# Kernel optimization log

Measured on AMD Instinct MI355X. Metric: run time of the kernel, lower is better.

Reference implementation:

```python
import jax, jax.numpy as jnp
import numpy as np

P, IMG, CH, DM, NL = 16, 224, 3, 512, 6
DI, N, K, R = 2 * DM, 16, 4, DM // 16  # d_inner, d_state, d_conv, dt_rank
BATCH = 32
L = (IMG // P) ** 2
PD = CH * P * P


def layernorm(x, g, b, eps=1e-5):
    mu = x.mean(-1, keepdims=True)
    var = x.var(-1, keepdims=True)
    return (x - mu) / jnp.sqrt(var + eps) * g + b


def mamba_layer(x, inW, convW, convB, xpW, dtW, dtB, A_log, Dvec, outW):
    # x: (B, L, DM)
    Bsz, Ls, _ = x.shape
    xz = x @ inW.T                      # (B, L, 2*DI), in_proj (bias=False)
    xs, z = jnp.split(xz, 2, axis=-1)   # (B, L, DI) each
    # causal depthwise conv1d (kernel K, left pad K-1, truncate to L)
    xp = jnp.pad(xs, ((0, 0), (K - 1, 0), (0, 0)))
    xc = sum(convW[:, k] * xp[:, k:k + Ls, :] for k in range(K)) + convB
    xc = jax.nn.silu(xc)
    # input-dependent dt, B, C
    x_dbl = xc @ xpW.T                  # (B, L, R + 2N)
    dt, Bm, Cm = jnp.split(x_dbl, [R, R + N], axis=-1)
    dt = jax.nn.softplus(dt @ dtW.T + dtB)  # (B, L, DI)
    A = -jnp.exp(A_log)                 # (DI, N)

    def step(h, inp):
        xt, dtt, Bt, Ct = inp           # (B,DI),(B,DI),(B,N),(B,N)
        dA = jnp.exp(dtt[:, :, None] * A)              # (B, DI, N)
        h = dA * h + dtt[:, :, None] * Bt[:, None, :] * xt[:, :, None]
        y = jnp.einsum('bdn,bn->bd', h, Ct)
        return h, y

    h0 = jnp.zeros((Bsz, DI, N), xs.dtype)
    xs_t = jnp.swapaxes(xc, 0, 1)
    dt_t = jnp.swapaxes(dt, 0, 1)
    B_t = jnp.swapaxes(Bm, 0, 1)
    C_t = jnp.swapaxes(Cm, 0, 1)
    _, ys = jax.lax.scan(step, h0, (xs_t, dt_t, B_t, C_t))
    y = jnp.swapaxes(ys, 0, 1) + xc * Dvec   # skip term D*x
    y = y * jax.nn.silu(z)
    return y @ outW.T                    # out_proj (bias=False)


def setup_inputs() -> dict:
    key = jax.random.key(0)
    ks = jax.random.split(key, 16)
    s = 0.02
    inp = {
        'x': jax.random.normal(ks[0], (BATCH, CH, IMG, IMG), jnp.float32),
        'ln0_g': jnp.ones((PD,), jnp.float32),
        'ln0_b': jnp.zeros((PD,), jnp.float32),
        'W_emb': jax.random.normal(ks[1], (DM, PD), jnp.float32) * s,
        'b_emb': jnp.zeros((DM,), jnp.float32),
        'ln1_g': jnp.ones((DM,), jnp.float32),
        'ln1_b': jnp.zeros((DM,), jnp.float32),
        'in_proj_w': jax.random.normal(ks[2], (NL, 2 * DI, DM), jnp.float32) * s,
        'conv_w': jax.random.normal(ks[3], (NL, DI, K), jnp.float32) * 0.1,
        'conv_b': jnp.zeros((NL, DI), jnp.float32),
        'x_proj_w': jax.random.normal(ks[4], (NL, R + 2 * N, DI), jnp.float32) * s,
        'dt_proj_w': jax.random.normal(ks[5], (NL, DI, R), jnp.float32) * s,
        'dt_proj_b': jnp.full((NL, DI), float(np.log(np.expm1(0.01))), jnp.float32),
        'A_log': jnp.tile(jnp.log(jnp.arange(1, N + 1, dtype=jnp.float32)), (NL, DI, 1)),
        'D_p': jnp.ones((NL, DI), jnp.float32),
        'out_proj_w': jax.random.normal(ks[6], (NL, DM, DI), jnp.float32) * s,
        'blk_ln_g': jnp.ones((NL, DM), jnp.float32),
        'blk_ln_b': jnp.zeros((NL, DM), jnp.float32),
        'W_head': jax.random.normal(ks[7], (10, DM), jnp.float32) * s,
        'b_head': jnp.zeros((10,), jnp.float32),
    }
    return inp


def reference(x, ln0_g, ln0_b, W_emb, b_emb, ln1_g, ln1_b, in_proj_w, conv_w,
              conv_b, x_proj_w, dt_proj_w, dt_proj_b, A_log, D_p, out_proj_w,
              blk_ln_g, blk_ln_b, W_head, b_head):
    B = x.shape[0]
    # patchify: b c (h p1) (w p2) -> b (h w) (c p1 p2)
    g = IMG // P
    t = x.reshape(B, CH, g, P, g, P).transpose(0, 2, 4, 1, 3, 5).reshape(B, g * g, PD)
    t = layernorm(t, ln0_g, ln0_b)
    t = t @ W_emb.T + b_emb
    t = layernorm(t, ln1_g, ln1_b)
    for i in range(NL):
        y = mamba_layer(t, in_proj_w[i], conv_w[i], conv_b[i], x_proj_w[i],
                        dt_proj_w[i], dt_proj_b[i], A_log[i], D_p[i], out_proj_w[i])
        t = layernorm(y + t, blk_ln_g[i], blk_ln_b[i])
    pooled = t.mean(axis=1)
    return pooled @ W_head.T + b_head
```

## Files before the change

kernel.cpp:

```cpp
#include <hip/hip_runtime.h>
#include <cstdint>
#include <cstddef>

#define BATCHN 32
#define LSEQ   196
#define DMODEL 512
#define DINNER 1024
#define PDIM   768
#define NSTATE 16
#define RRANK  32
#define NLAYER 6

typedef __bf16 bf16_t;
typedef __bf16 bf16x8 __attribute__((ext_vector_type(8)));
typedef float  f32x4  __attribute__((ext_vector_type(4)));

__device__ __forceinline__ void gl_lds16(const bf16_t* g, bf16_t* l) {
    __builtin_amdgcn_global_load_lds(
        (const __attribute__((address_space(1))) void*)g,
        (__attribute__((address_space(3))) void*)l, 16, 0, 0);
}

__global__ __launch_bounds__(256) void split_kernel(
    const float* __restrict__ src, bf16_t* __restrict__ hi,
    bf16_t* __restrict__ lo, int n)
{
    int i = blockIdx.x * 256 + threadIdx.x;
    if (i < n) {
        float x = src[i];
        bf16_t h = (bf16_t)x;
        hi[i] = h;
        lo[i] = (bf16_t)(x - (float)h);
    }
}

__global__ __launch_bounds__(256) void gemm_mfma3(
    const bf16_t* __restrict__ Ah, const bf16_t* __restrict__ Al,
    const bf16_t* __restrict__ Wh, const bf16_t* __restrict__ Wl,
    float* __restrict__ C, const float* __restrict__ bias,
    int M, int N, int K)
{
    __shared__ bf16_t sAh[128 * 32];
    __shared__ bf16_t sAl[128 * 32];
    __shared__ bf16_t sBh[128 * 32];
    __shared__ bf16_t sBl[128 * 32];

    const int bm = blockIdx.y * 128;
    const int bn = blockIdx.x * 128;
    const int tid  = threadIdx.x;
    const int lane = tid & 63;
    const int w    = tid >> 6;
    const int wm   = (w & 1) * 64;
    const int wn   = (w >> 1) * 64;

    const int lrow = lane >> 2;
    const int cg8  = ((lane & 3) ^ ((lane >> 3) & 3)) * 8;
    const size_t arow = (size_t)(bm + w * 32 + lrow) * K + cg8;
    const size_t brow = (size_t)(bn + w * 32 + lrow) * K + cg8;

    const int fsw = ((lane >> 4) ^ ((lane >> 1) & 3)) * 8;
    const int fr  = lane & 15;

    f32x4 acc[4][4] = {};

    for (int k0 = 0; k0 < K; k0 += 32) {
        __syncthreads();
        #pragma unroll
        for (int j = 0; j < 2; ++j) {
            const size_t ga = arow + (size_t)j * 16 * K + k0;
            const size_t gb = brow + (size_t)j * 16 * K + k0;
            const int lo = w * 1024 + j * 512;
            gl_lds16(Ah + ga, &sAh[lo]);
            gl_lds16(Al + ga, &sAl[lo]);
            gl_lds16(Wh + gb, &sBh[lo]);
            gl_lds16(Wl + gb, &sBl[lo]);
        }
        __syncthreads();

        bf16x8 afh[4], afl[4];
        #pragma unroll
        for (int mt = 0; mt < 4; ++mt) {
            const int r = wm + mt * 16 + fr;
            afh[mt] = *(const bf16x8*)&sAh[r * 32 + fsw];
            afl[mt] = *(const bf16x8*)&sAl[r * 32 + fsw];
        }
        #pragma unroll
        for (int nt = 0; nt < 4; ++nt) {
            const int r = wn + nt * 16 + fr;
            bf16x8 bfh = *(const bf16x8*)&sBh[r * 32 + fsw];
            bf16x8 bfl = *(const bf16x8*)&sBl[r * 32 + fsw];
            #pragma unroll
            for (int mt = 0; mt < 4; ++mt) {
                acc[mt][nt] = __builtin_amdgcn_mfma_f32_16x16x32_bf16(
                    afh[mt], bfh, acc[mt][nt], 0, 0, 0);
                acc[mt][nt] = __builtin_amdgcn_mfma_f32_16x16x32_bf16(
                    afh[mt], bfl, acc[mt][nt], 0, 0, 0);
                acc[mt][nt] = __builtin_amdgcn_mfma_f32_16x16x32_bf16(
                    afl[mt], bfh, acc[mt][nt], 0, 0, 0);
            }
        }
    }

    const int cr = (lane >> 4) * 4;
    const int cc = lane & 15;
    #pragma unroll
    for (int nt = 0; nt < 4; ++nt) {
        const int n = bn + wn + nt * 16 + cc;
        const float bv = bias ? bias[n] : 0.f;
        #pragma unroll
        for (int mt = 0; mt < 4; ++mt) {
            const int m0 = bm + wm + mt * 16 + cr;
            #pragma unroll
            for (int r = 0; r < 4; ++r)
                C[(size_t)(m0 + r) * N + n] = acc[mt][nt][r] + bv;
        }
    }
}

__global__ __launch_bounds__(256) void gemm_nt(
    const float* __restrict__ A, int lda,
    const float* __restrict__ W,
    float* __restrict__ C, int ldc,
    const float* __restrict__ bias,
    int M, int N, int K, int act)
{
    __shared__ float As[16][64];
    __shared__ float Ws[16][64];
    const int bm = blockIdx.y * 64;
    const int bn = blockIdx.x * 64;
    const int tid = threadIdx.x;
    const int tx = tid & 15;
    const int ty = tid >> 4;
    const int r   = tid >> 2;
    const int kk4 = (tid & 3) << 2;

    float acc[4][4];
    #pragma unroll
    for (int i = 0; i < 4; ++i)
        #pragma unroll
        for (int j = 0; j < 4; ++j) acc[i][j] = 0.f;

    for (int k0 = 0; k0 < K; k0 += 16) {
        float4 va = *(const float4*)(A + (size_t)(bm + r) * lda + k0 + kk4);
        float4 vw = *(const float4*)(W + (size_t)(bn + r) * K   + k0 + kk4);
        __syncthreads();
        As[kk4 + 0][r] = va.x; As[kk4 + 1][r] = va.y;
        As[kk4 + 2][r] = va.z; As[kk4 + 3][r] = va.w;
        Ws[kk4 + 0][r] = vw.x; Ws[kk4 + 1][r] = vw.y;
        Ws[kk4 + 2][r] = vw.z; Ws[kk4 + 3][r] = vw.w;
        __syncthreads();
        #pragma unroll
        for (int kk = 0; kk < 16; ++kk) {
            float4 a = *(const float4*)&As[kk][ty << 2];
            float4 b = *(const float4*)&Ws[kk][tx << 2];
            acc[0][0] += a.x * b.x; acc[0][1] += a.x * b.y;
            acc[0][2] += a.x * b.z; acc[0][3] += a.x * b.w;
            acc[1][0] += a.y * b.x; acc[1][1] += a.y * b.y;
            acc[1][2] += a.y * b.z; acc[1][3] += a.y * b.w;
            acc[2][0] += a.z * b.x; acc[2][1] += a.z * b.y;
            acc[2][2] += a.z * b.z; acc[2][3] += a.z * b.w;
            acc[3][0] += a.w * b.x; acc[3][1] += a.w * b.y;
            acc[3][2] += a.w * b.z; acc[3][3] += a.w * b.w;
        }
    }

    #pragma unroll
    for (int i = 0; i < 4; ++i) {
        const int m = bm + (ty << 2) + i;
        #pragma unroll
        for (int j = 0; j < 4; ++j) {
            const int n = bn + (tx << 2) + j;
            float v = acc[i][j];
            if (bias) v += bias[n];
            if (act == 1) {
                v = (v > 20.f) ? v : log1pf(expf(v));
            }
            C[(size_t)m * ldc + n] = v;
        }
    }
}

__global__ __launch_bounds__(256) void gemm_nt_splitk(
    const float* __restrict__ A, int lda,
    const float* __restrict__ W, int ldw,
    float* __restrict__ Cpart, int ldc,
    int M, int N, int kchunk)
{
    __shared__ float As[16][64];
    __shared__ float Ws[16][64];
    const int bm = blockIdx.y * 64;
    const int bn = blockIdx.x * 64;
    const int kb = blockIdx.z * kchunk;
    Cpart += (size_t)blockIdx.z * M * ldc;

    const int tid = threadIdx.x;
    const int tx = tid & 15;
    const int ty = tid >> 4;
    const int r   = tid >> 2;
    const int kk4 = (tid & 3) << 2;

    float acc[4][4];
    #pragma unroll
    for (int i = 0; i < 4; ++i)
        #pragma unroll
        for (int j = 0; j < 4; ++j) acc[i][j] = 0.f;

    for (int k0 = kb; k0 < kb + kchunk; k0 += 16) {
        float4 va = *(const float4*)(A + (size_t)(bm + r) * lda + k0 + kk4);
        float4 vw = *(const float4*)(W + (size_t)(bn + r) * ldw + k0 + kk4);
        __syncthreads();
        As[kk4 + 0][r] = va.x; As[kk4 + 1][r] = va.y;
        As[kk4 + 2][r] = va.z; As[kk4 + 3][r] = va.w;
        Ws[kk4 + 0][r] = vw.x; Ws[kk4 + 1][r] = vw.y;
        Ws[kk4 + 2][r] = vw.z; Ws[kk4 + 3][r] = vw.w;
        __syncthreads();
        #pragma unroll
        for (int kk = 0; kk < 16; ++kk) {
            float4 a = *(const float4*)&As[kk][ty << 2];
            float4 b = *(const float4*)&Ws[kk][tx << 2];
            acc[0][0] += a.x * b.x; acc[0][1] += a.x * b.y;
            acc[0][2] += a.x * b.z; acc[0][3] += a.x * b.w;
            acc[1][0] += a.y * b.x; acc[1][1] += a.y * b.y;
            acc[1][2] += a.y * b.z; acc[1][3] += a.y * b.w;
            acc[2][0] += a.z * b.x; acc[2][1] += a.z * b.y;
            acc[2][2] += a.z * b.z; acc[2][3] += a.z * b.w;
            acc[3][0] += a.w * b.x; acc[3][1] += a.w * b.y;
            acc[3][2] += a.w * b.z; acc[3][3] += a.w * b.w;
        }
    }

    #pragma unroll
    for (int i = 0; i < 4; ++i) {
        const int m = bm + (ty << 2) + i;
        #pragma unroll
        for (int j = 0; j < 4; ++j) {
            const int n = bn + (tx << 2) + j;
            Cpart[(size_t)m * ldc + n] = acc[i][j];
        }
    }
}

__global__ __launch_bounds__(256) void reduce_splitk(
    const float* __restrict__ part, float* __restrict__ out, int n, int nsplit)
{
    int i = blockIdx.x * 256 + threadIdx.x;
    if (i < n) {
        float s = 0.f;
        for (int j = 0; j < nsplit; ++j) s += part[(size_t)j * n + i];
        out[i] = s;
    }
}

__global__ __launch_bounds__(256) void patchify_kernel(
    const float* __restrict__ x, float* __restrict__ tp)
{
    int idx = blockIdx.x * 256 + threadIdx.x;
    int pd = idx % PDIM;
    int bl = idx / PDIM;
    int l = bl % LSEQ, b = bl / LSEQ;
    int c = pd >> 8, rem = pd & 255, p1 = rem >> 4, p2 = rem & 15;
    int gh = l / 14, gw = l % 14;
    int hh = gh * 16 + p1, ww = gw * 16 + p2;
    tp[idx] = x[(((size_t)b * 3 + c) * 224 + hh) * 224 + ww];
}

__global__ __launch_bounds__(256) void ln_kernel(
    const float* __restrict__ in, const float* __restrict__ res,
    const float* __restrict__ g, const float* __restrict__ bt,
    float* __restrict__ out, bf16_t* __restrict__ hi,
    bf16_t* __restrict__ lo, int W)
{
    __shared__ float red[4];
    const int row = blockIdx.x;
    const size_t base = (size_t)row * W;
    const int nper = W >> 8;
    float vals[3];
    float s = 0.f;
    for (int j = 0; j < nper; ++j) {
        int c = (j << 8) + threadIdx.x;
        float v = in[base + c];
        if (res) v += res[base + c];
        vals[j] = v;
        s += v;
    }
    int lane = threadIdx.x & 63, wid = threadIdx.x >> 6;
    #pragma unroll
    for (int o = 32; o > 0; o >>= 1) s += __shfl_down(s, o);
    if (lane == 0) red[wid] = s;
    __syncthreads();
    float mu = (red[0] + red[1] + red[2] + red[3]) / (float)W;
    __syncthreads();
    float vs = 0.f;
    for (int j = 0; j < nper; ++j) { float d = vals[j] - mu; vs += d * d; }
    #pragma unroll
    for (int o = 32; o > 0; o >>= 1) vs += __shfl_down(vs, o);
    if (lane == 0) red[wid] = vs;
    __syncthreads();
    float var = (red[0] + red[1] + red[2] + red[3]) / (float)W;
    float rstd = rsqrtf(var + 1e-5f);
    for (int j = 0; j < nper; ++j) {
        int c = (j << 8) + threadIdx.x;
        float v = (vals[j] - mu) * rstd * g[c] + bt[c];
        if (out) out[base + c] = v;
        if (hi) {
            bf16_t h = (bf16_t)v;
            hi[base + c] = h;
            lo[base + c] = (bf16_t)(v - (float)h);
        }
    }
}

__global__ __launch_bounds__(256) void conv_silu_kernel(
    const float* __restrict__ xz, const float* __restrict__ cw,
    const float* __restrict__ cb, float* __restrict__ xc)
{
    int idx = blockIdx.x * 256 + threadIdx.x;
    int d4 = idx & 255;
    int bl = idx >> 8;
    int l = bl % LSEQ, b = bl / LSEQ;
    int d = d4 << 2;

    float4 w0 = *(const float4*)(cw + (size_t)(d + 0) * 4);
    float4 w1 = *(const float4*)(cw + (size_t)(d + 1) * 4);
    float4 w2 = *(const float4*)(cw + (size_t)(d + 2) * 4);
    float4 w3 = *(const float4*)(cw + (size_t)(d + 3) * 4);
    float4 acc = *(const float4*)(cb + d);

    const float* base = xz + ((size_t)(b * LSEQ) << 11) + d;
    #pragma unroll
    for (int k = 0; k < 4; ++k) {
        int ls = l + k - 3;
        if (ls >= 0) {
            float4 xv = *(const float4*)(base + ((size_t)ls << 11));
            const float wk0 = (&w0.x)[k], wk1 = (&w1.x)[k];
            const float wk2 = (&w2.x)[k], wk3 = (&w3.x)[k];
            acc.x += wk0 * xv.x; acc.y += wk1 * xv.y;
            acc.z += wk2 * xv.z; acc.w += wk3 * xv.w;
        }
    }
    acc.x = acc.x * __builtin_amdgcn_rcpf(1.f + __expf(-acc.x));
    acc.y = acc.y * __builtin_amdgcn_rcpf(1.f + __expf(-acc.y));
    acc.z = acc.z * __builtin_amdgcn_rcpf(1.f + __expf(-acc.z));
    acc.w = acc.w * __builtin_amdgcn_rcpf(1.f + __expf(-acc.w));
    *(float4*)(xc + ((size_t)bl << 10) + d) = acc;
}

template<int J>
__device__ __forceinline__ float qbcast(float v) {
    constexpr int ctrl = J | (J << 2) | (J << 4) | (J << 6);
    return __int_as_float(__builtin_amdgcn_mov_dpp(
        __float_as_int(v), ctrl, 0xF, 0xF, true));
}

__global__ __launch_bounds__(256, 1) void scan_kernel(
    const float* __restrict__ xc, const float* __restrict__ dt,
    const float* __restrict__ xdbl, const float* __restrict__ A_log,
    const float* __restrict__ Dv, const float* __restrict__ xz,
    bf16_t* __restrict__ yh, bf16_t* __restrict__ yl)
{
    __shared__ float sBC[4][2][256];

    const int b    = blockIdx.y;
    const int tid  = threadIdx.x;
    const int lane = tid & 63;
    const int w    = tid >> 6;
    const int q    = tid >> 2;
    const int sub  = tid & 3;
    const int d    = blockIdx.x * 64 + q;

    float A2[4], h[4];
    #pragma unroll
    for (int n = 0; n < 4; ++n) {
        A2[n] = -__expf(A_log[d * NSTATE + sub * 4 + n]) * 1.44269504f;
        h[n] = 0.f;
    }
    const float Dval = Dv[d];
    const size_t bL = (size_t)b * LSEQ;

    const float* pdt = dt + (bL + sub) * DINNER + d;
    const float* pxc = xc + (bL + sub) * DINNER + d;
    const float* pz  = xz + ((bL + sub) << 11) + DINNER + d;

    const float* xrow = xdbl + bL * 64;
    const int roff = (lane >> 4) * 64 + (lane & 15) * 4;
    float* lds0 = &sBC[w][0][0];
    float* lds1 = &sBC[w][1][0];

    float4 r0 = *(const float4*)(xrow + roff);
    float4 r1 = *(const float4*)(xrow + 256 + roff);
    float4 rowreg = *(const float4*)(xrow + 512 + roff);
    *(float4*)(lds0 + roff) = r0;
    *(float4*)(lds1 + roff) = r1;

    float dt_c = pdt[0];          float xc_c = pxc[0];          float z_c = pz[0];
    float dt_1 = pdt[4 * DINNER]; float xc_1 = pxc[4 * DINNER]; float z_1 = pz[4 * 2048];

    for (int g = 0; g < 49; ++g) {
        const int gl  = (g + 3 <= 48) ? g + 3 : 48;
        float4 rownext = *(const float4*)(xrow + gl * 256 + roff);
        const int adv = (g < 47) ? 2 : (48 - g);
        float dt_2 = pdt[(size_t)adv * 4 * DINNER];
        float xc_2 = pxc[(size_t)adv * 4 * DINNER];
        float z_2  = pz[(size_t)adv * 4 * 2048];

        const float* Bbuf = (g & 1) ? lds1 : lds0;
        float acc_keep = 0.f;

#define SCAN_STEP(J) do {                                                     \
        float4 Bv = *(const float4*)&Bbuf[(J) * 64 + 32 + 4 * sub];           \
        float4 Cv = *(const float4*)&Bbuf[(J) * 64 + 48 + 4 * sub];           \
        float dtv = qbcast<J>(dt_c);                                          \
        float xv  = qbcast<J>(xc_c);                                          \
        float dtx = dtv * xv;                                                 \
        h[0] = exp2f(dtv * A2[0]) * h[0] + dtx * Bv.x;                        \
        h[1] = exp2f(dtv * A2[1]) * h[1] + dtx * Bv.y;                        \
        h[2] = exp2f(dtv * A2[2]) * h[2] + dtx * Bv.z;                        \
        h[3] = exp2f(dtv * A2[3]) * h[3] + dtx * Bv.w;                        \
        float acc = h[0] * Cv.x + h[1] * Cv.y + h[2] * Cv.z + h[3] * Cv.w;    \
        acc += __shfl_xor(acc, 1);                                            \
        acc += __shfl_xor(acc, 2);                                            \
        acc_keep = (sub == (J)) ? acc : acc_keep;                             \
    } while (0)

        SCAN_STEP(0);
        SCAN_STEP(1);
        SCAN_STEP(2);
        SCAN_STEP(3);
#undef SCAN_STEP

        {
            float yv = acc_keep + xc_c * Dval;
            float sz = z_c * __builtin_amdgcn_rcpf(1.f + __expf(-z_c));
            float o  = yv * sz;
            bf16_t ho = (bf16_t)o;
            const size_t oi = (bL + 4 * (size_t)g + sub) * DINNER + d;
            yh[oi] = ho;
            yl[oi] = (bf16_t)(o - (float)ho);
        }

        *(float4*)(((g & 1) ? lds1 : lds0) + roff) = rowreg;
        rowreg = rownext;

        pdt += 4 * DINNER; pxc += 4 * DINNER; pz += 4 * 2048;
        dt_c = dt_1; xc_c = xc_1; z_c = z_1;
        dt_1 = dt_2; xc_1 = xc_2; z_1 = z_2;
    }
}

__global__ __launch_bounds__(256) void pool_kernel(
    const float* __restrict__ t, float* __restrict__ pooled)
{
    int idx = blockIdx.x * 256 + threadIdx.x;
    int dm = idx & (DMODEL - 1);
    int b = idx >> 9;
    float s = 0.f;
    for (int l = 0; l < LSEQ; ++l)
        s += t[((size_t)(b * LSEQ + l) << 9) + dm];
    pooled[idx] = s * (1.f / (float)LSEQ);
}

__global__ __launch_bounds__(320) void head_kernel(
    const float* __restrict__ pooled, const float* __restrict__ Wh,
    const float* __restrict__ bh, float* __restrict__ out)
{
    int tid = threadIdx.x;
    if (tid >= 320) return;
    int b = tid / 10, o = tid % 10;
    float s = bh[o];
    for (int k = 0; k < DMODEL; ++k)
        s += pooled[b * DMODEL + k] * Wh[o * DMODEL + k];
    out[b * 10 + o] = s;
}

extern "C" void kernel_launch(void* const* d_in, const int* in_sizes, int n_in,
                              void* d_out, int out_size, void* d_ws, size_t ws_size,
                              hipStream_t stream)
{
    const float* x         = (const float*)d_in[0];
    const float* ln0_g     = (const float*)d_in[1];
    const float* ln0_b     = (const float*)d_in[2];
    const float* W_emb     = (const float*)d_in[3];
    const float* b_emb     = (const float*)d_in[4];
    const float* ln1_g     = (const float*)d_in[5];
    const float* ln1_b     = (const float*)d_in[6];
    const float* in_proj_w = (const float*)d_in[7];
    const float* conv_w    = (const float*)d_in[8];
    const float* conv_b    = (const float*)d_in[9];
    const float* x_proj_w  = (const float*)d_in[10];
    const float* dt_proj_w = (const float*)d_in[11];
    const float* dt_proj_b = (const float*)d_in[12];
    const float* A_log     = (const float*)d_in[13];
    const float* D_p       = (const float*)d_in[14];
    const float* out_proj_w= (const float*)d_in[15];
    const float* blk_ln_g  = (const float*)d_in[16];
    const float* blk_ln_b  = (const float*)d_in[17];
    const float* W_head    = (const float*)d_in[18];
    const float* b_head    = (const float*)d_in[19];

    const int M = BATCHN * LSEQ;
    const int NSPLIT = 8;

    char* ws = (char*)d_ws;
    size_t off = 0;
    auto alloc = [&](size_t bytes) -> void* {
        void* p = (void*)(ws + off);
        off += (bytes + 255) & ~(size_t)255;
        return p;
    };
    float*  tp     = (float*)alloc((size_t)M * PDIM * 4);
    bf16_t* tp_h   = (bf16_t*)alloc((size_t)M * PDIM * 2);
    bf16_t* tp_l   = (bf16_t*)alloc((size_t)M * PDIM * 2);
    float*  t      = (float*)alloc((size_t)M * DMODEL * 4);
    bf16_t* t_h    = (bf16_t*)alloc((size_t)M * DMODEL * 2);
    bf16_t* t_l    = (bf16_t*)alloc((size_t)M * DMODEL * 2);
    float*  xz     = (float*)alloc((size_t)M * 2 * DINNER * 4);
    float*  xc     = (float*)alloc((size_t)M * DINNER * 4);
    float*  xdbl   = (float*)alloc((size_t)M * 64 * 4);
    float*  xdbl_p = (float*)alloc((size_t)NSPLIT * M * 64 * 4);
    float*  dtbuf  = (float*)alloc((size_t)M * DINNER * 4);
    bf16_t* y_h    = (bf16_t*)alloc((size_t)M * DINNER * 2);
    bf16_t* y_l    = (bf16_t*)alloc((size_t)M * DINNER * 2);
    float*  yout   = (float*)alloc((size_t)M * DMODEL * 4);
    float*  pooled = (float*)alloc((size_t)BATCHN * DMODEL * 4);
    const int n_inW  = NLAYER * 2 * DINNER * DMODEL;
    const int n_outW = NLAYER * DMODEL * DINNER;
    const int n_embW = DMODEL * PDIM;
    bf16_t* winh  = (bf16_t*)alloc((size_t)n_inW * 2);
    bf16_t* winl  = (bf16_t*)alloc((size_t)n_inW * 2);
    bf16_t* wouth = (bf16_t*)alloc((size_t)n_outW * 2);
    bf16_t* woutl = (bf16_t*)alloc((size_t)n_outW * 2);
    bf16_t* wembh = (bf16_t*)alloc((size_t)n_embW * 2);
    bf16_t* wembl = (bf16_t*)alloc((size_t)n_embW * 2);
    (void)ws_size; (void)in_sizes; (void)n_in; (void)out_size;

    split_kernel<<<(n_inW  + 255) / 256, 256, 0, stream>>>(in_proj_w,  winh,  winl,  n_inW);
    split_kernel<<<(n_outW + 255) / 256, 256, 0, stream>>>(out_proj_w, wouth, woutl, n_outW);
    split_kernel<<<(n_embW + 255) / 256, 256, 0, stream>>>(W_emb,      wembh, wembl, n_embW);

    patchify_kernel<<<(M * PDIM) / 256, 256, 0, stream>>>(x, tp);
    ln_kernel<<<M, 256, 0, stream>>>(tp, nullptr, ln0_g, ln0_b, nullptr, tp_h, tp_l, PDIM);
    gemm_mfma3<<<dim3(DMODEL / 128, M / 128), 256, 0, stream>>>(
        tp_h, tp_l, wembh, wembl, t, b_emb, M, DMODEL, PDIM);
    ln_kernel<<<M, 256, 0, stream>>>(t, nullptr, ln1_g, ln1_b, t, t_h, t_l, DMODEL);

    for (int i = 0; i < NLAYER; ++i) {
        const bf16_t* winh_i  = winh  + (size_t)i * 2 * DINNER * DMODEL;
        const bf16_t* winl_i  = winl  + (size_t)i * 2 * DINNER * DMODEL;
        const bf16_t* wouth_i = wouth + (size_t)i * DMODEL * DINNER;
        const bf16_t* woutl_i = woutl + (size_t)i * DMODEL * DINNER;
        const float* cw   = conv_w    + (size_t)i * DINNER * 4;
        const float* cb   = conv_b    + (size_t)i * DINNER;
        const float* xpW  = x_proj_w  + (size_t)i * 64 * DINNER;
        const float* dtW  = dt_proj_w + (size_t)i * DINNER * RRANK;
        const float* dtB  = dt_proj_b + (size_t)i * DINNER;
        const float* Ali  = A_log     + (size_t)i * DINNER * NSTATE;
        const float* Di   = D_p       + (size_t)i * DINNER;
        const float* bg   = blk_ln_g  + (size_t)i * DMODEL;
        const float* bb   = blk_ln_b  + (size_t)i * DMODEL;

        gemm_mfma3<<<dim3((2 * DINNER) / 128, M / 128), 256, 0, stream>>>(
            t_h, t_l, winh_i, winl_i, xz, nullptr, M, 2 * DINNER, DMODEL);
        conv_silu_kernel<<<(M * DINNER / 4) / 256, 256, 0, stream>>>(xz, cw, cb, xc);
        gemm_nt_splitk<<<dim3(1, M / 64, NSPLIT), 256, 0, stream>>>(
            xc, DINNER, xpW, DINNER, xdbl_p, 64, M, 64, DINNER / NSPLIT);
        reduce_splitk<<<(M * 64 + 255) / 256, 256, 0, stream>>>(
            xdbl_p, xdbl, M * 64, NSPLIT);
        gemm_nt<<<dim3(DINNER / 64, M / 64), 256, 0, stream>>>(
            xdbl, 64, dtW, dtbuf, DINNER, dtB, M, DINNER, RRANK, 1);
        scan_kernel<<<dim3(DINNER / 64, BATCHN), 256, 0, stream>>>(
            xc, dtbuf, xdbl, Ali, Di, xz, y_h, y_l);
        gemm_mfma3<<<dim3(DMODEL / 128, M / 128), 256, 0, stream>>>(
            y_h, y_l, wouth_i, woutl_i, yout, nullptr, M, DMODEL, DINNER);
        ln_kernel<<<M, 256, 0, stream>>>(yout, t, bg, bb, t, t_h, t_l, DMODEL);
    }

    pool_kernel<<<(BATCHN * DMODEL) / 256, 256, 0, stream>>>(t, pooled);
    head_kernel<<<1, 320, 0, stream>>>(pooled, W_head, b_head, (float*)d_out);
}
```

Baseline: 1.697 ms.

## Fuse conv into x_proj, split-K out_proj, double-buffer GEMM B tiles

Merges the causal depthwise conv and SiLU into the split-K x_proj GEMM, which removes a separate kernel launch and one reread of xc. The out_proj GEMM now runs split-K over two z-slices, and the following layernorm sums the two partial outputs. The MFMA GEMM double-buffers only its weight tiles in LDS while the A tiles stay single-buffered behind an extra barrier. Buffers are aliased (xdbl_p onto tp, yout onto dtbuf) to save memory; the aliasing and the partially double-buffered pipeline carry correctness risk.

```diff
diff --git a/kernel.cpp b/kernel.cpp
--- a/kernel.cpp
+++ b/kernel.cpp
@@ -42,11 +42,15 @@
 {
     __shared__ bf16_t sAh[128 * 32];
     __shared__ bf16_t sAl[128 * 32];
-    __shared__ bf16_t sBh[128 * 32];
-    __shared__ bf16_t sBl[128 * 32];
+    __shared__ bf16_t sBh[2][128 * 32];
+    __shared__ bf16_t sBl[2][128 * 32];
 
     const int bm = blockIdx.y * 128;
     const int bn = blockIdx.x * 128;
+    const int kchunk = K / gridDim.z;
+    const int kb = blockIdx.z * kchunk;
+    C += (size_t)blockIdx.z * M * N;
+
     const int tid  = threadIdx.x;
     const int lane = tid & 63;
     const int w    = tid >> 6;
@@ -60,21 +64,21 @@
 
     const int fsw = ((lane >> 4) ^ ((lane >> 1) & 3)) * 8;
     const int fr  = lane & 15;
+    const int llo = w * 1024;
 
     f32x4 acc[4][4] = {};
 
-    for (int k0 = 0; k0 < K; k0 += 32) {
-        __syncthreads();
-        #pragma unroll
-        for (int j = 0; j < 2; ++j) {
-            const size_t ga = arow + (size_t)j * 16 * K + k0;
-            const size_t gb = brow + (size_t)j * 16 * K + k0;
-            const int lo = w * 1024 + j * 512;
-            gl_lds16(Ah + ga, &sAh[lo]);
-            gl_lds16(Al + ga, &sAl[lo]);
-            gl_lds16(Wh + gb, &sBh[lo]);
-            gl_lds16(Wl + gb, &sBl[lo]);
-        }
+    #pragma unroll
+    for (int j = 0; j < 2; ++j) {
+        gl_lds16(Ah + arow + (size_t)j * 16 * K + kb, &sAh[llo + j * 512]);
+        gl_lds16(Al + arow + (size_t)j * 16 * K + kb, &sAl[llo + j * 512]);
+        gl_lds16(Wh + brow + (size_t)j * 16 * K + kb, &sBh[0][llo + j * 512]);
+        gl_lds16(Wl + brow + (size_t)j * 16 * K + kb, &sBl[0][llo + j * 512]);
+    }
+
+    const int kiter = kchunk / 32;
+    for (int ki = 0; ki < kiter; ++ki) {
+        const int buf = ki & 1;
         __syncthreads();
 
         bf16x8 afh[4], afl[4];
@@ -84,11 +88,24 @@
             afh[mt] = *(const bf16x8*)&sAh[r * 32 + fsw];
             afl[mt] = *(const bf16x8*)&sAl[r * 32 + fsw];
         }
+        __syncthreads();
+
+        if (ki + 1 < kiter) {
+            const int k0 = kb + (ki + 1) * 32;
+            #pragma unroll
+            for (int j = 0; j < 2; ++j) {
+                gl_lds16(Ah + arow + (size_t)j * 16 * K + k0, &sAh[llo + j * 512]);
+                gl_lds16(Al + arow + (size_t)j * 16 * K + k0, &sAl[llo + j * 512]);
+                gl_lds16(Wh + brow + (size_t)j * 16 * K + k0, &sBh[buf ^ 1][llo + j * 512]);
+                gl_lds16(Wl + brow + (size_t)j * 16 * K + k0, &sBl[buf ^ 1][llo + j * 512]);
+            }
+        }
+
         #pragma unroll
         for (int nt = 0; nt < 4; ++nt) {
             const int r = wn + nt * 16 + fr;
-            bf16x8 bfh = *(const bf16x8*)&sBh[r * 32 + fsw];
-            bf16x8 bfl = *(const bf16x8*)&sBl[r * 32 + fsw];
+            bf16x8 bfh = *(const bf16x8*)&sBh[buf][r * 32 + fsw];
+            bf16x8 bfl = *(const bf16x8*)&sBl[buf][r * 32 + fsw];
             #pragma unroll
             for (int mt = 0; mt < 4; ++mt) {
                 acc[mt][nt] = __builtin_amdgcn_mfma_f32_16x16x32_bf16(
@@ -180,24 +197,34 @@
     }
 }
 
-__global__ __launch_bounds__(256) void gemm_nt_splitk(
-    const float* __restrict__ A, int lda,
-    const float* __restrict__ W, int ldw,
-    float* __restrict__ Cpart, int ldc,
-    int M, int N, int kchunk)
+__global__ __launch_bounds__(256) void conv_xproj_kernel(
+    const float* __restrict__ xz, const float* __restrict__ cw,
+    const float* __restrict__ cb, const float* __restrict__ xpW,
+    float* __restrict__ xc, float* __restrict__ Cpart,
+    int kchunk)
 {
     __shared__ float As[16][64];
     __shared__ float Ws[16][64];
+    __shared__ float scw[128 * 4 + 128];
+
     const int bm = blockIdx.y * 64;
-    const int bn = blockIdx.x * 64;
     const int kb = blockIdx.z * kchunk;
-    Cpart += (size_t)blockIdx.z * M * ldc;
+    Cpart += (size_t)blockIdx.z * (BATCHN * LSEQ) * 64;
 
     const int tid = threadIdx.x;
+    if (tid < 128) {
+        *(float4*)&scw[tid * 4] = *(const float4*)(cw + (size_t)(kb + tid) * 4);
+        scw[512 + tid] = cb[kb + tid];
+    }
+    __syncthreads();
+
     const int tx = tid & 15;
     const int ty = tid >> 4;
     const int r   = tid >> 2;
     const int kk4 = (tid & 3) << 2;
+    const int bl  = bm + r;
+    const int l   = bl % LSEQ;
+    const float* xrow = xz + ((size_t)bl << 11);
 
     float acc[4][4];
     #pragma unroll
@@ -205,9 +232,28 @@
         #pragma unroll
         for (int j = 0; j < 4; ++j) acc[i][j] = 0.f;
 
-    for (int k0 = kb; k0 < kb + kchunk; k0 += 16) {
-        float4 va = *(const float4*)(A + (size_t)(bm + r) * lda + k0 + kk4);
-        float4 vw = *(const float4*)(W + (size_t)(bn + r) * ldw + k0 + kk4);
+    for (int k0 = 0; k0 < kchunk; k0 += 16) {
+        const int cl = k0 + kk4;
+        const int c  = kb + cl;
+        float4 va = *(const float4*)&scw[512 + cl];
+        #pragma unroll
+        for (int kk = 0; kk < 4; ++kk) {
+            int ls = l + kk - 3;
+            if (ls >= 0) {
+                float4 xv = *(const float4*)(xrow + ((ptrdiff_t)(kk - 3) << 11) + c);
+                va.x += scw[(cl + 0) * 4 + kk] * xv.x;
+                va.y += scw[(cl + 1) * 4 + kk] * xv.y;
+                va.z += scw[(cl + 2) * 4 + kk] * xv.z;
+                va.w += scw[(cl + 3) * 4 + kk] * xv.w;
+            }
+        }
+        va.x = va.x * __builtin_amdgcn_rcpf(1.f + __expf(-va.x));
+        va.y = va.y * __builtin_amdgcn_rcpf(1.f + __expf(-va.y));
+        va.z = va.z * __builtin_amdgcn_rcpf(1.f + __expf(-va.z));
+        va.w = va.w * __builtin_amdgcn_rcpf(1.f + __expf(-va.w));
+        *(float4*)(xc + ((size_t)bl << 10) + c) = va;
+
+        float4 vw = *(const float4*)(xpW + (size_t)r * DINNER + c);
         __syncthreads();
         As[kk4 + 0][r] = va.x; As[kk4 + 1][r] = va.y;
         As[kk4 + 2][r] = va.z; As[kk4 + 3][r] = va.w;
@@ -234,8 +280,8 @@
         const int m = bm + (ty << 2) + i;
         #pragma unroll
         for (int j = 0; j < 4; ++j) {
-            const int n = bn + (tx << 2) + j;
-            Cpart[(size_t)m * ldc + n] = acc[i][j];
+            const int n = (tx << 2) + j;
+            Cpart[(size_t)m * 64 + n] = acc[i][j];
         }
     }
 }
@@ -265,7 +311,8 @@
 }
 
 __global__ __launch_bounds__(256) void ln_kernel(
-    const float* __restrict__ in, const float* __restrict__ res,
+    const float* __restrict__ in, const float* __restrict__ in2,
+    const float* __restrict__ res,
     const float* __restrict__ g, const float* __restrict__ bt,
     float* __restrict__ out, bf16_t* __restrict__ hi,
     bf16_t* __restrict__ lo, int W)
@@ -279,6 +326,7 @@
     for (int j = 0; j < nper; ++j) {
         int c = (j << 8) + threadIdx.x;
         float v = in[base + c];
+        if (in2) v += in2[base + c];
         if (res) v += res[base + c];
         vals[j] = v;
         s += v;
@@ -308,41 +356,6 @@
             lo[base + c] = (bf16_t)(v - (float)h);
         }
     }
-}
-
-__global__ __launch_bounds__(256) void conv_silu_kernel(
-    const float* __restrict__ xz, const float* __restrict__ cw,
-    const float* __restrict__ cb, float* __restrict__ xc)
-{
-    int idx = blockIdx.x * 256 + threadIdx.x;
-    int d4 = idx & 255;
-    int bl = idx >> 8;
-    int l = bl % LSEQ, b = bl / LSEQ;
-    int d = d4 << 2;
-
-    float4 w0 = *(const float4*)(cw + (size_t)(d + 0) * 4);
-    float4 w1 = *(const float4*)(cw + (size_t)(d + 1) * 4);
-    float4 w2 = *(const float4*)(cw + (size_t)(d + 2) * 4);
-    float4 w3 = *(const float4*)(cw + (size_t)(d + 3) * 4);
-    float4 acc = *(const float4*)(cb + d);
-
-    const float* base = xz + ((size_t)(b * LSEQ) << 11) + d;
-    #pragma unroll
-    for (int k = 0; k < 4; ++k) {
-        int ls = l + k - 3;
-        if (ls >= 0) {
-            float4 xv = *(const float4*)(base + ((size_t)ls << 11));
-            const float wk0 = (&w0.x)[k], wk1 = (&w1.x)[k];
-            const float wk2 = (&w2.x)[k], wk3 = (&w3.x)[k];
-            acc.x += wk0 * xv.x; acc.y += wk1 * xv.y;
-            acc.z += wk2 * xv.z; acc.w += wk3 * xv.w;
-        }
-    }
-    acc.x = acc.x * __builtin_amdgcn_rcpf(1.f + __expf(-acc.x));
-    acc.y = acc.y * __builtin_amdgcn_rcpf(1.f + __expf(-acc.y));
-    acc.z = acc.z * __builtin_amdgcn_rcpf(1.f + __expf(-acc.z));
-    acc.w = acc.w * __builtin_amdgcn_rcpf(1.f + __expf(-acc.w));
-    *(float4*)(xc + ((size_t)bl << 10) + d) = acc;
 }
 
 template<int J>
@@ -516,12 +529,12 @@
     float*  xz     = (float*)alloc((size_t)M * 2 * DINNER * 4);
     float*  xc     = (float*)alloc((size_t)M * DINNER * 4);
     float*  xdbl   = (float*)alloc((size_t)M * 64 * 4);
-    float*  xdbl_p = (float*)alloc((size_t)NSPLIT * M * 64 * 4);
     float*  dtbuf  = (float*)alloc((size_t)M * DINNER * 4);
     bf16_t* y_h    = (bf16_t*)alloc((size_t)M * DINNER * 2);
     bf16_t* y_l    = (bf16_t*)alloc((size_t)M * DINNER * 2);
-    float*  yout   = (float*)alloc((size_t)M * DMODEL * 4);
     float*  pooled = (float*)alloc((size_t)BATCHN * DMODEL * 4);
+    float*  xdbl_p = tp;
+    float*  yout   = dtbuf;
     const int n_inW  = NLAYER * 2 * DINNER * DMODEL;
     const int n_outW = NLAYER * DMODEL * DINNER;
     const int n_embW = DMODEL * PDIM;
@@ -538,10 +551,12 @@
     split_kernel<<<(n_embW + 255) / 256, 256, 0, stream>>>(W_emb,      wembh, wembl, n_embW);
 
     patchify_kernel<<<(M * PDIM) / 256, 256, 0, stream>>>(x, tp);
-    ln_kernel<<<M, 256, 0, stream>>>(tp, nullptr, ln0_g, ln0_b, nullptr, tp_h, tp_l, PDIM);
-    gemm_mfma3<<<dim3(DMODEL / 128, M / 128), 256, 0, stream>>>(
+    ln_kernel<<<M, 256, 0, stream>>>(tp, nullptr, nullptr, ln0_g, ln0_b,
+                                     nullptr, tp_h, tp_l, PDIM);
+    gemm_mfma3<<<dim3(DMODEL / 128, M / 128, 1), 256, 0, stream>>>(
         tp_h, tp_l, wembh, wembl, t, b_emb, M, DMODEL, PDIM);
-    ln_kernel<<<M, 256, 0, stream>>>(t, nullptr, ln1_g, ln1_b, t, t_h, t_l, DMODEL);
+    ln_kernel<<<M, 256, 0, stream>>>(t, nullptr, nullptr, ln1_g, ln1_b,
+                                     t, t_h, t_l, DMODEL);
 
     for (int i = 0; i < NLAYER; ++i) {
         const bf16_t* winh_i  = winh  + (size_t)i * 2 * DINNER * DMODEL;
@@ -558,20 +573,20 @@
         const float* bg   = blk_ln_g  + (size_t)i * DMODEL;
         const float* bb   = blk_ln_b  + (size_t)i * DMODEL;
 
-        gemm_mfma3<<<dim3((2 * DINNER) / 128, M / 128), 256, 0, stream>>>(
+        gemm_mfma3<<<dim3((2 * DINNER) / 128, M / 128, 1), 256, 0, stream>>>(
             t_h, t_l, winh_i, winl_i, xz, nullptr, M, 2 * DINNER, DMODEL);
-        conv_silu_kernel<<<(M * DINNER / 4) / 256, 256, 0, stream>>>(xz, cw, cb, xc);
-        gemm_nt_splitk<<<dim3(1, M / 64, NSPLIT), 256, 0, stream>>>(
-            xc, DINNER, xpW, DINNER, xdbl_p, 64, M, 64, DINNER / NSPLIT);
+        conv_xproj_kernel<<<dim3(1, M / 64, NSPLIT), 256, 0, stream>>>(
+            xz, cw, cb, xpW, xc, xdbl_p, DINNER / NSPLIT);
         reduce_splitk<<<(M * 64 + 255) / 256, 256, 0, stream>>>(
             xdbl_p, xdbl, M * 64, NSPLIT);
         gemm_nt<<<dim3(DINNER / 64, M / 64), 256, 0, stream>>>(
             xdbl, 64, dtW, dtbuf, DINNER, dtB, M, DINNER, RRANK, 1);
         scan_kernel<<<dim3(DINNER / 64, BATCHN), 256, 0, stream>>>(
             xc, dtbuf, xdbl, Ali, Di, xz, y_h, y_l);
-        gemm_mfma3<<<dim3(DMODEL / 128, M / 128), 256, 0, stream>>>(
+        gemm_mfma3<<<dim3(DMODEL / 128, M / 128, 2), 256, 0, stream>>>(
             y_h, y_l, wouth_i, woutl_i, yout, nullptr, M, DMODEL, DINNER);
-        ln_kernel<<<M, 256, 0, stream>>>(yout, t, bg, bb, t, t_h, t_l, DMODEL);
+        ln_kernel<<<M, 256, 0, stream>>>(yout, yout + (size_t)M * DMODEL, t,
+                                         bg, bb, t, t_h, t_l, DMODEL);
     }
 
     pool_kernel<<<(BATCHN * DMODEL) / 256, 256, 0, stream>>>(t, pooled);
```

Measured after the change: 1.544 ms. 9.0% less time.
